# Performance work log

Measured on AMD Instinct MI355X. Metric: run time of the kernel, lower is better.

The kernel has to match this reference:

```python
import jax, jax.numpy as jnp
import numpy as np

N = 131072  # total sentences
D = 768     # relation/sentence embedding dim
B = 16384   # number of bags (scopes)
C = 53      # n_class (NYT10 relations)


def setup_inputs() -> dict:
    key = jax.random.key(0)
    k1, k2, k3, k4, k5 = jax.random.split(key, 5)
    x = jax.random.normal(k1, (N, D), dtype=jnp.float32)
    label = jax.random.randint(k2, (N,), 0, C)              # per-sentence bag label
    segment_ids = jnp.sort(jax.random.randint(k3, (N,), 0, B))  # sorted -> contiguous scopes
    rel_weight = jax.random.normal(k4, (C, D), dtype=jnp.float32) * 0.05  # relation_matrix.weight
    bias = jax.random.normal(k5, (C,), dtype=jnp.float32)
    return {"x": x, "label": label, "segment_ids": segment_ids,
            "rel_weight": rel_weight, "bias": bias}


def reference(x, label, segment_ids, rel_weight, bias):
    # _attention_train_logit: <x_i, relation_matrix[label_i]>  -> [N]
    att = jnp.sum(x * rel_weight[label], axis=1)
    # per-bag (segment) stable softmax over sentences in each scope
    seg_max = jax.ops.segment_max(att, segment_ids, num_segments=B)      # [B]
    e = jnp.exp(att - seg_max[segment_ids])                              # [N]
    denom = jax.ops.segment_sum(e, segment_ids, num_segments=B)         # [B]
    # softmax-weighted pooling: sum_i softmax_i * x_i per bag
    num = jax.ops.segment_sum(e[:, None] * x, segment_ids, num_segments=B)  # [B, D]
    repre = num / jnp.where(denom == 0, 1.0, denom)[:, None]
    # get_logits (dropout=0.0 -> identity)
    logits = repre @ rel_weight.T + bias                                 # [B, C]
    return logits
```

## Files before the change

kernel.cpp:

```cpp
#include <hip/hip_runtime.h>
#include <math.h>

#define DN  768
#define NC  53
#define NCP 64
#define NKS 24
#define MB  256
#define YTS 66

typedef __attribute__((ext_vector_type(8))) __bf16 bf16x8;
typedef __attribute__((ext_vector_type(8))) short short8v;
typedef __attribute__((ext_vector_type(4))) float f32x4;

static __device__ __forceinline__ unsigned short f2bf(float f) {
    unsigned int u = __builtin_bit_cast(unsigned int, f);
    u = (u + 0x7FFFu + ((u >> 16) & 1u)) >> 16;
    return (unsigned short)u;
}
static __device__ __forceinline__ float bf2f(unsigned short h) {
    unsigned int u = ((unsigned int)h) << 16;
    return __builtin_bit_cast(float, u);
}

__global__ void prep_kernel(const float* __restrict__ w,
                            const int*   __restrict__ seg,
                            unsigned short* __restrict__ wb,
                            int* __restrict__ offs,
                            int N, int B) {
    const int bid = blockIdx.x;
    if (bid < 192) {
        int i = bid * 256 + threadIdx.x;
        const int e    = i & 7;
        const int lane = (i >> 3) & 63;
        const int ct   = (i >> 9) & 3;
        const int ks   = i >> 11;
        const int cls  = ct * 16 + (lane & 15);
        const int k    = ks * 32 + ((lane >> 4) << 3) + e;
        wb[i] = (cls < NC) ? f2bf(w[cls * DN + k]) : (unsigned short)0;
    } else {
        int i = (bid - 192) * 256 + threadIdx.x;
        if (i >= N) return;
        int cur  = seg[i];
        int prev = (i == 0) ? -1 : seg[i - 1];
        for (int b = prev + 1; b <= cur; ++b) offs[b] = i;
        if (i == N - 1)
            for (int b = cur + 1; b <= B; ++b) offs[b] = N;
    }
}

#define ISSUE(buf, ks)                                                         \
    {                                                                          \
        _Pragma("unroll")                                                      \
        for (int f = 0; f < 4; ++f) {                                          \
            const float* ap = a0 + (size_t)f * 16 * DN + (ks) * 32;            \
            la[buf][f * 2]     = *(const float4*)(ap);                         \
            la[buf][f * 2 + 1] = *(const float4*)(ap + 4);                     \
        }                                                                      \
        _Pragma("unroll")                                                      \
        for (int ct = 0; ct < 4; ++ct)                                         \
            lb[buf][ct] = *(const short8v*)(wb + (((ks) * 4 + ct) * 64 + lane) * 8); \
    }

__global__ __launch_bounds__(256) void gemm_y3(
    const float* __restrict__ x,
    const int*   __restrict__ label,
    const unsigned short* __restrict__ wb,
    unsigned short* __restrict__ yb,
    float* __restrict__ att)
{
    __shared__ float yt[4][64 * YTS];

    const int lane = threadIdx.x & 63;
    const int wv   = threadIdx.x >> 6;
    const int r16  = lane & 15;
    const int kg   = lane >> 4;
    const long row0 = (long)blockIdx.x * MB + wv * 64;

    f32x4 acc[4][4];
    #pragma unroll
    for (int f = 0; f < 4; ++f)
        #pragma unroll
        for (int ct = 0; ct < 4; ++ct)
            acc[f][ct] = (f32x4){0.f, 0.f, 0.f, 0.f};

    const float* a0 = x + (row0 + r16) * DN + kg * 8;

    float4  la[2][8];
    short8v lb[2][4];
    ISSUE(0, 0)

    #pragma unroll
    for (int ks = 0; ks < NKS; ++ks) {
        const int cur = ks & 1, nxt = cur ^ 1;
        if (ks + 1 < NKS) ISSUE(nxt, ks + 1)

        short8v a8[4];
        #pragma unroll
        for (int f = 0; f < 4; ++f) {
            const float4 u0 = la[cur][f * 2], u1 = la[cur][f * 2 + 1];
            short8v t;
            t[0] = (short)f2bf(u0.x); t[1] = (short)f2bf(u0.y);
            t[2] = (short)f2bf(u0.z); t[3] = (short)f2bf(u0.w);
            t[4] = (short)f2bf(u1.x); t[5] = (short)f2bf(u1.y);
            t[6] = (short)f2bf(u1.z); t[7] = (short)f2bf(u1.w);
            a8[f] = t;
        }
        #pragma unroll
        for (int ct = 0; ct < 4; ++ct)
            #pragma unroll
            for (int f = 0; f < 4; ++f)
                acc[f][ct] = __builtin_amdgcn_mfma_f32_16x16x32_bf16(
                    __builtin_bit_cast(bf16x8, a8[f]),
                    __builtin_bit_cast(bf16x8, lb[cur][ct]), acc[f][ct], 0, 0, 0);
    }

    float* myt = yt[wv];
    #pragma unroll
    for (int f = 0; f < 4; ++f)
        #pragma unroll
        for (int ct = 0; ct < 4; ++ct) {
            const int rl = f * 16 + kg * 4;
            #pragma unroll
            for (int r = 0; r < 4; ++r) {
                const float v = acc[f][ct][r];
                myt[(rl + r) * YTS + ct * 16 + r16] = v;
                yb[(row0 + rl + r) * NCP + ct * 16 + r16] = f2bf(v);
            }
        }
    {
        const long grow = row0 + lane;
        const int  lab  = label[grow];
        att[grow] = myt[lane * YTS + lab];
    }
}

__global__ __launch_bounds__(256) void pool_kernel(
    const unsigned short* __restrict__ yb,
    const float* __restrict__ att,
    const int*   __restrict__ offs,
    const float* __restrict__ bias,
    float*       __restrict__ out,
    int Btot)
{
    __shared__ float s_e[4][64];
    const int wv   = threadIdx.x >> 6;
    const int lane = threadIdx.x & 63;
    const int bag  = blockIdx.x * 4 + wv;
    if (bag >= Btot) return;
    const int s = offs[bag], e = offs[bag + 1];

    float m = -INFINITY, den = 0.f, facc = 0.f;
    for (int j0 = s; j0 < e; j0 += 64) {
        const int j = j0 + lane;
        float a = (j < e) ? att[j] : -INFINITY;
        float cm = a;
        #pragma unroll
        for (int off = 1; off < 64; off <<= 1) cm = fmaxf(cm, __shfl_xor(cm, off));
        const float nm = fmaxf(m, cm);
        const float sc = __expf(m - nm);
        const float ej = (j < e) ? __expf(a - nm) : 0.f;
        float cd = ej;
        #pragma unroll
        for (int off = 1; off < 64; off <<= 1) cd += __shfl_xor(cd, off);
        den = den * sc + cd;
        s_e[wv][lane] = ej;
        const int cnt = min(64, e - j0);
        float f0 = 0.f, f1 = 0.f, f2 = 0.f, f3 = 0.f;
        int t = 0;
        for (; t + 4 <= cnt; t += 4) {
            f0 += s_e[wv][t]     * bf2f(yb[(size_t)(j0 + t)     * NCP + lane]);
            f1 += s_e[wv][t + 1] * bf2f(yb[(size_t)(j0 + t + 1) * NCP + lane]);
            f2 += s_e[wv][t + 2] * bf2f(yb[(size_t)(j0 + t + 2) * NCP + lane]);
            f3 += s_e[wv][t + 3] * bf2f(yb[(size_t)(j0 + t + 3) * NCP + lane]);
        }
        for (; t < cnt; ++t)
            f0 += s_e[wv][t] * bf2f(yb[(size_t)(j0 + t) * NCP + lane]);
        facc = facc * sc + ((f0 + f1) + (f2 + f3));
        m = nm;
    }
    if (lane < NC) {
        const float inv = (den == 0.f) ? 0.f : 1.f / den;
        out[(size_t)bag * NC + lane] = facc * inv + bias[lane];
    }
}

extern "C" void kernel_launch(void* const* d_in, const int* in_sizes, int n_in,
                              void* d_out, int out_size, void* d_ws, size_t ws_size,
                              hipStream_t stream)
{
    const float* x     = (const float*)d_in[0];
    const int*   label = (const int*)  d_in[1];
    const int*   seg   = (const int*)  d_in[2];
    const float* w     = (const float*)d_in[3];
    const float* bias  = (const float*)d_in[4];
    float*       out   = (float*)d_out;

    const int N = in_sizes[0] / DN;
    const int B = out_size / NC;

    unsigned short* wb   = (unsigned short*)d_ws;
    int*            offs = (int*)((char*)d_ws + 131072);
    float*          att  = (float*)((char*)d_ws + 1048576);
    unsigned short* yb   = (unsigned short*)((char*)d_ws + 2097152);

    hipLaunchKernelGGL(prep_kernel, dim3(192 + (N + 255) / 256), dim3(256), 0, stream,
                       w, seg, wb, offs, N, B);
    hipLaunchKernelGGL(gemm_y3, dim3(N / MB), dim3(256), 0, stream,
                       x, label, wb, yb, att);
    hipLaunchKernelGGL(pool_kernel, dim3((B + 3) / 4), dim3(256), 0, stream,
                       yb, att, offs, bias, out, B);
}
```

Baseline: 113.5 us.

## Stage x through LDS with async global_load_lds and smaller row blocks

The GEMM kernel is restructured. Each wave now handles 16 rows instead of 64 and blocks cover 64 rows, so the grid is four times larger. Activations are copied straight into swizzled double-buffered LDS with global_load_lds in 128-column chunks, replacing register-held prefetch, with manual vmcnt waits to overlap the loads with MFMA. This aims to raise occupancy and memory-level parallelism on the bandwidth-bound read of x. In exchange it adds LDS pressure, reloads the weight fragments more often per row, and reads att from a bf16-rounded value instead of fp32, which costs a little accuracy.

```diff
diff --git a/kernel.cpp b/kernel.cpp
--- a/kernel.cpp
+++ b/kernel.cpp
@@ -1,12 +1,11 @@
 #include <hip/hip_runtime.h>
 #include <math.h>
 
-#define DN  768
-#define NC  53
-#define NCP 64
-#define NKS 24
-#define MB  256
-#define YTS 66
+#define DN   768
+#define NC   53
+#define NCP  64
+#define NKC  6
+#define MBLK 64
 
 typedef __attribute__((ext_vector_type(8))) __bf16 bf16x8;
 typedef __attribute__((ext_vector_type(8))) short short8v;
@@ -21,6 +20,11 @@
     unsigned int u = ((unsigned int)h) << 16;
     return __builtin_bit_cast(float, u);
 }
+
+#define GLOAD16(gptr, lptr)                                        \
+    __builtin_amdgcn_global_load_lds(                              \
+        (const __attribute__((address_space(1))) void*)(gptr),     \
+        (__attribute__((address_space(3))) void*)(lptr), 16, 0, 0)
 
 __global__ void prep_kernel(const float* __restrict__ w,
                             const int*   __restrict__ seg,
@@ -48,89 +52,101 @@
     }
 }
 
-#define ISSUE(buf, ks)                                                         \
-    {                                                                          \
-        _Pragma("unroll")                                                      \
-        for (int f = 0; f < 4; ++f) {                                          \
-            const float* ap = a0 + (size_t)f * 16 * DN + (ks) * 32;            \
-            la[buf][f * 2]     = *(const float4*)(ap);                         \
-            la[buf][f * 2 + 1] = *(const float4*)(ap + 4);                     \
-        }                                                                      \
-        _Pragma("unroll")                                                      \
-        for (int ct = 0; ct < 4; ++ct)                                         \
-            lb[buf][ct] = *(const short8v*)(wb + (((ks) * 4 + ct) * 64 + lane) * 8); \
-    }
-
-__global__ __launch_bounds__(256) void gemm_y3(
+__global__ __launch_bounds__(256) void gemm_y5(
     const float* __restrict__ x,
     const int*   __restrict__ label,
     const unsigned short* __restrict__ wb,
     unsigned short* __restrict__ yb,
     float* __restrict__ att)
 {
-    __shared__ float yt[4][64 * YTS];
+    __shared__ float          xs[2][4][16][128];
+    __shared__ unsigned short yt[4][16][66];
 
     const int lane = threadIdx.x & 63;
     const int wv   = threadIdx.x >> 6;
     const int r16  = lane & 15;
     const int kg   = lane >> 4;
-    const long row0 = (long)blockIdx.x * MB + wv * 64;
-
-    f32x4 acc[4][4];
+    const long row0w = (long)blockIdx.x * MBLK + wv * 16;
+
+    f32x4 acc[4];
     #pragma unroll
-    for (int f = 0; f < 4; ++f)
-        #pragma unroll
-        for (int ct = 0; ct < 4; ++ct)
-            acc[f][ct] = (f32x4){0.f, 0.f, 0.f, 0.f};
-
-    const float* a0 = x + (row0 + r16) * DN + kg * 8;
-
-    float4  la[2][8];
-    short8v lb[2][4];
-    ISSUE(0, 0)
+    for (int ct = 0; ct < 4; ++ct) acc[ct] = (f32x4){0.f, 0.f, 0.f, 0.f};
+
+    const int srowp = lane >> 5;
+    const int sgs   = lane & 31;
+    char* const xsb = (char*)xs;
+
+    short8v lb[2][4][4];
+
+#define ISSUE_LB(buf, ch)                                                      \
+    {                                                                          \
+        _Pragma("unroll")                                                      \
+        for (int ks = 0; ks < 4; ++ks)                                         \
+            _Pragma("unroll")                                                  \
+            for (int ct = 0; ct < 4; ++ct)                                     \
+                lb[buf][ks][ct] = *(const short8v*)(                           \
+                    wb + ((((ch) * 4 + ks) * 4 + ct) * 64 + lane) * 8);        \
+    }
+
+#define STAGE(buf, ch)                                                         \
+    {                                                                          \
+        _Pragma("unroll")                                                      \
+        for (int i = 0; i < 8; ++i) {                                          \
+            const int rl = 2 * i + srowp;                                      \
+            const int gx = sgs ^ (rl & 7);         \
+            const float* sp = x + (row0w + rl) * (long)DN + (ch) * 128 + gx * 4;\
+            char* lp = xsb + (buf) * 32768 + wv * 8192 + i * 1024; \
+            GLOAD16(sp, lp);                                                   \
+        }                                                                      \
+    }
+
+    ISSUE_LB(0, 0)
+    STAGE(0, 0)
 
     #pragma unroll
-    for (int ks = 0; ks < NKS; ++ks) {
-        const int cur = ks & 1, nxt = cur ^ 1;
-        if (ks + 1 < NKS) ISSUE(nxt, ks + 1)
-
-        short8v a8[4];
-        #pragma unroll
-        for (int f = 0; f < 4; ++f) {
-            const float4 u0 = la[cur][f * 2], u1 = la[cur][f * 2 + 1];
-            short8v t;
-            t[0] = (short)f2bf(u0.x); t[1] = (short)f2bf(u0.y);
-            t[2] = (short)f2bf(u0.z); t[3] = (short)f2bf(u0.w);
-            t[4] = (short)f2bf(u1.x); t[5] = (short)f2bf(u1.y);
-            t[6] = (short)f2bf(u1.z); t[7] = (short)f2bf(u1.w);
-            a8[f] = t;
-        }
-        #pragma unroll
-        for (int ct = 0; ct < 4; ++ct)
+    for (int ch = 0; ch < NKC; ++ch) {
+        const int cur = ch & 1, nxt = cur ^ 1;
+        if (ch + 1 < NKC) {
+            ISSUE_LB(nxt, ch + 1)
+            STAGE(nxt, ch + 1)
+            asm volatile("s_waitcnt vmcnt(24)" ::: "memory");
+        } else {
+            asm volatile("s_waitcnt vmcnt(0)" ::: "memory");
+        }
+        #pragma unroll
+        for (int ks = 0; ks < 4; ++ks) {
+            const char* base = xsb + cur * 32768 + wv * 8192 + r16 * 512;
+            const int g0 = ks * 8 + kg * 2;
+            const float4 u0 = *(const float4*)(base + ((g0    ) ^ (r16 & 7)) * 16);
+            const float4 u1 = *(const float4*)(base + ((g0 + 1) ^ (r16 & 7)) * 16);
+            bf16x8 a8;
+            a8[0] = (__bf16)u0.x; a8[1] = (__bf16)u0.y;
+            a8[2] = (__bf16)u0.z; a8[3] = (__bf16)u0.w;
+            a8[4] = (__bf16)u1.x; a8[5] = (__bf16)u1.y;
+            a8[6] = (__bf16)u1.z; a8[7] = (__bf16)u1.w;
             #pragma unroll
-            for (int f = 0; f < 4; ++f)
-                acc[f][ct] = __builtin_amdgcn_mfma_f32_16x16x32_bf16(
-                    __builtin_bit_cast(bf16x8, a8[f]),
-                    __builtin_bit_cast(bf16x8, lb[cur][ct]), acc[f][ct], 0, 0, 0);
-    }
-
-    float* myt = yt[wv];
+            for (int ct = 0; ct < 4; ++ct)
+                acc[ct] = __builtin_amdgcn_mfma_f32_16x16x32_bf16(
+                    a8, __builtin_bit_cast(bf16x8, lb[cur][ks][ct]), acc[ct], 0, 0, 0);
+        }
+    }
+
+#undef ISSUE_LB
+#undef STAGE
+
     #pragma unroll
-    for (int f = 0; f < 4; ++f)
-        #pragma unroll
-        for (int ct = 0; ct < 4; ++ct) {
-            const int rl = f * 16 + kg * 4;
-            #pragma unroll
-            for (int r = 0; r < 4; ++r) {
-                const float v = acc[f][ct][r];
-                myt[(rl + r) * YTS + ct * 16 + r16] = v;
-                yb[(row0 + rl + r) * NCP + ct * 16 + r16] = f2bf(v);
-            }
-        }
-    {
-        const long grow = row0 + lane;
+    for (int ct = 0; ct < 4; ++ct)
+        #pragma unroll
+        for (int r = 0; r < 4; ++r) {
+            const int   rl = kg * 4 + r;
+            const float v  = acc[ct][r];
+            yb[(row0w + rl) * NCP + ct * 16 + r16] = f2bf(v);
+            yt[wv][rl][ct * 16 + r16] = f2bf(v);
+        }
+    if (lane < 16) {
+        const long grow = row0w + lane;
         const int  lab  = label[grow];
-        att[grow] = myt[lane * YTS + lab];
+        att[grow] = bf2f(yt[wv][lane][lab]);
     }
 }
 
@@ -205,7 +221,7 @@
 
     hipLaunchKernelGGL(prep_kernel, dim3(192 + (N + 255) / 256), dim3(256), 0, stream,
                        w, seg, wb, offs, N, B);
-    hipLaunchKernelGGL(gemm_y3, dim3(N / MB), dim3(256), 0, stream,
+    hipLaunchKernelGGL(gemm_y5, dim3(N / MBLK), dim3(256), 0, stream,
                        x, label, wb, yb, att);
     hipLaunchKernelGGL(pool_kernel, dim3((B + 3) / 4), dim3(256), 0, stream,
                        yb, att, offs, bias, out, B);
```

Result: faster. 110.4 us (-2.7%).
